# Performance work log

Hardware: AMD Instinct MI355X
Metric: run time of the kernel (lower is better)

The kernel has to match this reference:

```python
import jax, jax.numpy as jnp
import numpy as np

BETA = 0.25

def setup_inputs() -> dict:
    key = jax.random.key(0)
    k1, k2 = jax.random.split(key)
    x = jax.random.normal(k1, (32, 1024, 256), dtype=jnp.float32)
    # tf.random_uniform_initializer default range is [-0.05, 0.05)
    embedding = jax.random.uniform(k2, (256, 8192), dtype=jnp.float32, minval=-0.05, maxval=0.05)
    return {"x": x, "embedding": embedding}


def reference(x, embedding):
    # x: [B, S, D]; embedding: [D, K] (codebook stored column-wise, as in the tf module)
    D = x.shape[-1]
    flat = x.reshape(-1, D)                                   # [N, D]
    dists = (jnp.sum(flat * flat, axis=1, keepdims=True)
             - 2.0 * (flat @ embedding)
             + jnp.sum(embedding * embedding, axis=0))
    idx = jnp.argmin(dists, axis=1)                           # [N] int
    quantized = jnp.take(embedding.T, idx, axis=0).reshape(x.shape)  # gather codebook columns
    # VQ losses
    commitment = jnp.mean(jnp.square(jax.lax.stop_gradient(quantized) - x))
    codebook = jnp.mean(jnp.square(quantized - jax.lax.stop_gradient(x)))
    loss = BETA * commitment + codebook
    # straight-through estimator
    quantized_st = x + jax.lax.stop_gradient(quantized - x)
    return quantized_st, loss
```

## Files before the change

### kernel.cpp

```cpp
#include <hip/hip_runtime.h>

typedef float f4   __attribute__((ext_vector_type(4)));
typedef float f2   __attribute__((ext_vector_type(2)));
typedef _Float16 f16x8 __attribute__((ext_vector_type(8)));
typedef float f32x4  __attribute__((ext_vector_type(4)));

#define N_ROWS  32768
#define D_DIM   256
#define K_CODES 8192
#define NUM_ELEM (N_ROWS * D_DIM)
#define EPS_MARGIN 2e-3f
#define FB_CAP  8192
#define FB_RPB  8
#define RF_SLICES 16
#define N_PANELS 256
#define HALF_PANELS 128

__device__ __forceinline__ void gl2lds16(const void* g, void* l) {
    __builtin_amdgcn_global_load_lds(
        (const __attribute__((address_space(1))) unsigned int*)g,
        (__attribute__((address_space(3))) unsigned int*)l, 16, 0, 0);
}

__global__ void ee_kernel(const float* __restrict__ E, float* __restrict__ ee) {
    const int k = blockIdx.x * blockDim.x + threadIdx.x;
    double s = 0.0;
    for (int d = 0; d < D_DIM; ++d) {
        float v = E[(size_t)d * K_CODES + k];
        s += (double)v * (double)v;
    }
    ee[k] = (float)s;
}

__global__ void prep_kernel(const float* __restrict__ E, short* __restrict__ Ep) {
    const int p  = blockIdx.x;
    const int t  = threadIdx.x;
    const int c  = t & 31;
    const int gq = t >> 5;
    const int cp = p * 32;
    short* ph = Ep + (size_t)p * 8192;
    #pragma unroll
    for (int gi = 0; gi < 4; ++gi) {
        int g = gq * 4 + gi;
        f16x8 h;
        #pragma unroll
        for (int j = 0; j < 8; ++j) {
            float v = E[(size_t)(g * 8 + j) * K_CODES + cp + c];
            h[j] = (_Float16)v;
        }
        *(f16x8*)(ph + (g * 32 + c) * 8) = h;
    }
}

__global__ void trans32_kernel(const float* __restrict__ E, float* __restrict__ Et32) {
    __shared__ float tile[64][65];
    const int t  = threadIdx.x;
    const int k0 = blockIdx.x * 64, d0 = blockIdx.y * 64;
    #pragma unroll
    for (int i = 0; i < 16; ++i) {
        int dd = i * 4 + (t >> 6), kk = t & 63;
        tile[dd][kk] = E[(size_t)(d0 + dd) * K_CODES + k0 + kk];
    }
    __syncthreads();
    #pragma unroll
    for (int i = 0; i < 16; ++i) {
        int kk = i * 4 + (t >> 6), dd = t & 63;
        Et32[(size_t)(k0 + kk) * D_DIM + d0 + dd] = tile[dd][kk];
    }
}

__launch_bounds__(256, 2)
__global__ void mfma_sieve_kernel(const float* __restrict__ X,
                                  const short* __restrict__ Ep,
                                  const float* __restrict__ ee,
                                  f2* __restrict__ res_bs,
                                  int* __restrict__ res_idx) {
    __shared__ __align__(16) short Bbuf[2][8192];
    const int t    = threadIdx.x;
    const int w    = t >> 6;
    const int lane = t & 63;
    const int n    = lane & 15;
    const int quad = lane >> 4;
    const int half = blockIdx.x & 1;
    const int row0 = (blockIdx.x >> 1) * 128;
    const int rw   = row0 + w * 32;
    const int p0   = half * HALF_PANELS;

    f16x8 Ah[2][8];
    #pragma unroll
    for (int rt = 0; rt < 2; ++rt) {
        const float* xp = X + (size_t)(rw + rt * 16 + n) * D_DIM;
        #pragma unroll
        for (int ks = 0; ks < 8; ++ks) {
            int d = ks * 32 + quad * 8;
            f4 a = *(const f4*)(xp + d);
            f4 b = *(const f4*)(xp + d + 4);
            f16x8 h;
            #pragma unroll
            for (int j = 0; j < 8; ++j) {
                float x = (j < 4) ? a[j] : b[j - 4];
                h[j] = (_Float16)x;
            }
            Ah[rt][ks] = h;
        }
    }

    float bestv[8], secv[8]; int besti[8];
    #pragma unroll
    for (int s = 0; s < 8; ++s) { bestv[s] = 1e30f; secv[s] = 1e30f; besti[s] = 0; }

    {
        const char* gp = (const char*)Ep + (size_t)p0 * 16384;
        char* lp = (char*)&Bbuf[0][0];
        #pragma unroll
        for (int i = 0; i < 4; ++i)
            gl2lds16(gp + (w * 4 + i) * 1024 + lane * 16, lp + (w * 4 + i) * 1024);
    }
    __syncthreads();

    for (int i = 0; i < HALF_PANELS; ++i) {
        const int p   = p0 + i;
        const int buf = i & 1;
        if (i + 1 < HALF_PANELS) {
            const char* gp = (const char*)Ep + (size_t)(p + 1) * 16384;
            char* lp = (char*)&Bbuf[buf ^ 1][0];
            #pragma unroll
            for (int k = 0; k < 4; ++k)
                gl2lds16(gp + (w * 4 + k) * 1024 + lane * 16, lp + (w * 4 + k) * 1024);
        }

        const short* Bh = &Bbuf[buf][0];

        f32x4 acc[2][2];
        #pragma unroll
        for (int ct = 0; ct < 2; ++ct)
            #pragma unroll
            for (int rt = 0; rt < 2; ++rt)
                acc[ct][rt] = (f32x4)(0.0f);

        #pragma unroll
        for (int ks = 0; ks < 8; ++ks) {
            const int g = ks * 4 + quad;
            f16x8 bh[2];
            #pragma unroll
            for (int ct = 0; ct < 2; ++ct) {
                int c = ct * 16 + n;
                bh[ct] = *(const f16x8*)(Bh + (g * 32 + c) * 8);
            }
            #pragma unroll
            for (int ct = 0; ct < 2; ++ct)
                #pragma unroll
                for (int rt = 0; rt < 2; ++rt)
                    acc[ct][rt] = __builtin_amdgcn_mfma_f32_16x16x32_f16(Ah[rt][ks], bh[ct], acc[ct][rt], 0, 0, 0);
        }

        const int cb = p * 32;
        #pragma unroll
        for (int ct = 0; ct < 2; ++ct) {
            int code = cb + ct * 16 + n;
            float eev = ee[code];
            #pragma unroll
            for (int rt = 0; rt < 2; ++rt)
                #pragma unroll
                for (int r = 0; r < 4; ++r) {
                    float key = fmaf(-2.0f, acc[ct][rt][r], eev);
                    int s = rt * 4 + r;
                    float nb = fminf(key, bestv[s]);
                    secv[s]  = fminf(secv[s], fmaxf(key, bestv[s]));
                    besti[s] = (key < bestv[s]) ? code : besti[s];
                    bestv[s] = nb;
                }
        }
        __syncthreads();
    }

    #pragma unroll
    for (int off = 1; off < 16; off <<= 1) {
        #pragma unroll
        for (int s = 0; s < 8; ++s) {
            float ov = __shfl_xor(bestv[s], off);
            int   oi = __shfl_xor(besti[s], off);
            float os = __shfl_xor(secv[s], off);
            bool owin = (ov < bestv[s]) || (ov == bestv[s] && oi < besti[s]);
            if (owin) { secv[s] = fminf(os, bestv[s]); bestv[s] = ov; besti[s] = oi; }
            else      { secv[s] = fminf(secv[s], ov); }
        }
    }

    if (n == 0) {
        #pragma unroll
        for (int s = 0; s < 8; ++s) {
            int rl  = w * 32 + (s >> 2) * 16 + quad * 4 + (s & 3);
            int row = row0 + rl;
            f2 bs; bs[0] = bestv[s]; bs[1] = secv[s];
            res_bs[(size_t)row * 2 + half]  = bs;
            res_idx[(size_t)row * 2 + half] = besti[s];
        }
    }
}

__global__ void merge_kernel(const f2* __restrict__ res_bs, const int* __restrict__ res_idx,
                             int* __restrict__ bidx, int* __restrict__ counter,
                             int2* __restrict__ list) {
    const int row = blockIdx.x * blockDim.x + threadIdx.x;
    if (row >= N_ROWS) return;
    f2 a = res_bs[(size_t)row * 2];
    f2 b = res_bs[(size_t)row * 2 + 1];
    int ia = res_idx[(size_t)row * 2];
    int ib = res_idx[(size_t)row * 2 + 1];
    float gb; int gi; float gs;
    if (b[0] < a[0]) { gb = b[0]; gi = ib; gs = fminf(b[1], a[0]); }
    else             { gb = a[0]; gi = ia; gs = fminf(a[1], b[0]); }
    bidx[row] = gi;
    if (gs - gb <= EPS_MARGIN) {
        int pos = atomicAdd(counter, 1);
        if (pos < FB_CAP) list[pos] = make_int2(row, gi);
    }
}

__global__ void gather_kernel(const float* __restrict__ X, const float* __restrict__ Et32,
                              const int* __restrict__ bidx, float* __restrict__ out,
                              double* __restrict__ loss_sum) {
    __shared__ int bl_[128];
    const int t    = threadIdx.x;
    const int row0 = blockIdx.x * 128;
    if (t < 128) bl_[t] = bidx[row0 + t];
    __syncthreads();
    double ls = 0.0;
    const int d = t;
    #pragma unroll 4
    for (int r = 0; r < 128; ++r) {
        int code = bl_[r];
        float q  = Et32[(size_t)code * D_DIM + d];
        float x  = X[(size_t)(row0 + r) * D_DIM + d];
        float dq = q - x;
        out[(size_t)(row0 + r) * D_DIM + d] = x + dq;
        ls += (double)dq * (double)dq;
    }
    #pragma unroll
    for (int off = 32; off > 0; off >>= 1)
        ls += __shfl_down(ls, off);
    if ((t & 63) == 0) atomicAdd(loss_sum, ls);
}

__global__ void refine1_kernel(const float* __restrict__ X, const float* __restrict__ E,
                               const int* __restrict__ counter, const int2* __restrict__ list,
                               double* __restrict__ res_v, int* __restrict__ res_i) {
    __shared__ float xt[D_DIM][FB_RPB];
    __shared__ int rows_sh[FB_RPB];
    __shared__ double wbv[4][FB_RPB];
    __shared__ int    wbi[4][FB_RPB];

    int nf = *counter; if (nf > FB_CAP) nf = FB_CAP;
    const int nchunks = (nf + FB_RPB - 1) / FB_RPB;
    const int nitems  = nchunks * RF_SLICES;
    const int t = threadIdx.x;

    for (int item = blockIdx.x; item < nitems; item += gridDim.x) {
        const int rc = item / RF_SLICES;
        const int sl = item % RF_SLICES;
        __syncthreads();
        if (t < FB_RPB) {
            int e = rc * FB_RPB + t;
            int2 ent = list[(e < nf) ? e : 0];
            rows_sh[t] = ent.x;
        }
        __syncthreads();
        #pragma unroll
        for (int j = 0; j < FB_RPB; ++j)
            xt[t][j] = X[(size_t)rows_sh[j] * D_DIM + t];
        __syncthreads();

        const int k0 = sl * 512 + t * 2;
        double s0[FB_RPB], s1[FB_RPB], q0 = 0.0, q1 = 0.0;
        #pragma unroll
        for (int j = 0; j < FB_RPB; ++j) { s0[j] = 0.0; s1[j] = 0.0; }
        for (int d = 0; d < D_DIM; ++d) {
            f2 ev = *(const f2*)(E + (size_t)d * K_CODES + k0);
            double e0d = (double)ev[0], e1d = (double)ev[1];
            const f4* xp = (const f4*)(&xt[d][0]);
            f4 xa = xp[0], xb = xp[1];
            double xd[FB_RPB] = { (double)xa[0], (double)xa[1], (double)xa[2], (double)xa[3],
                                  (double)xb[0], (double)xb[1], (double)xb[2], (double)xb[3] };
            q0 += e0d * e0d; q1 += e1d * e1d;
            #pragma unroll
            for (int j = 0; j < FB_RPB; ++j) {
                s0[j] += xd[j] * e0d;
                s1[j] += xd[j] * e1d;
            }
        }
        double bv[FB_RPB]; int bi[FB_RPB];
        #pragma unroll
        for (int j = 0; j < FB_RPB; ++j) {
            double k0v = q0 - 2.0 * s0[j];
            double k1v = q1 - 2.0 * s1[j];
            bv[j] = k0v; bi[j] = k0;
            if (k1v < bv[j]) { bv[j] = k1v; bi[j] = k0 + 1; }
        }
        #pragma unroll
        for (int off = 1; off < 64; off <<= 1) {
            #pragma unroll
            for (int j = 0; j < FB_RPB; ++j) {
                double ov = __shfl_xor(bv[j], off);
                int    oi = __shfl_xor(bi[j], off);
                if (ov < bv[j] || (ov == bv[j] && oi < bi[j])) { bv[j] = ov; bi[j] = oi; }
            }
        }
        const int wave = t >> 6;
        if ((t & 63) == 0) {
            #pragma unroll
            for (int j = 0; j < FB_RPB; ++j) { wbv[wave][j] = bv[j]; wbi[wave][j] = bi[j]; }
        }
        __syncthreads();
        if (t < FB_RPB) {
            double b = wbv[0][t]; int i_ = wbi[0][t];
            #pragma unroll
            for (int wv = 1; wv < 4; ++wv) {
                double ov = wbv[wv][t]; int oi = wbi[wv][t];
                if (ov < b || (ov == b && oi < i_)) { b = ov; i_ = oi; }
            }
            int e = rc * FB_RPB + t;
            res_v[(size_t)e * RF_SLICES + sl] = b;
            res_i[(size_t)e * RF_SLICES + sl] = i_;
        }
    }
}

__global__ void patch_kernel(const float* __restrict__ X, const float* __restrict__ Et32,
                             float* __restrict__ out, double* __restrict__ loss_sum,
                             const int* __restrict__ counter, const int2* __restrict__ list,
                             const double* __restrict__ res_v, const int* __restrict__ res_i) {
    int nf = *counter; if (nf > FB_CAP) nf = FB_CAP;
    const int b = blockIdx.x;
    if (b >= nf) return;
    __shared__ int nc_sh;
    const int t = threadIdx.x;
    if (t == 0) {
        double bv = res_v[(size_t)b * RF_SLICES]; int bi = res_i[(size_t)b * RF_SLICES];
        for (int s = 1; s < RF_SLICES; ++s) {
            double v = res_v[(size_t)b * RF_SLICES + s];
            int    i = res_i[(size_t)b * RF_SLICES + s];
            if (v < bv || (v == bv && i < bi)) { bv = v; bi = i; }
        }
        nc_sh = bi;
    }
    __syncthreads();
    int2 ent = list[b];
    const int oc = ent.y, row = ent.x, nc = nc_sh;
    if (nc == oc) return;
    float x  = X[(size_t)row * D_DIM + t];
    float qn = Et32[(size_t)nc * D_DIM + t];
    float qo = Et32[(size_t)oc * D_DIM + t];
    float dqn = qn - x, dqo = qo - x;
    out[(size_t)row * D_DIM + t] = x + dqn;
    double dl = (double)dqn * dqn - (double)dqo * dqo;
    #pragma unroll
    for (int off = 32; off > 0; off >>= 1)
        dl += __shfl_down(dl, off);
    if ((t & 63) == 0) atomicAdd(loss_sum, dl);
}

__global__ void fin_kernel(const double* __restrict__ loss_sum, float* __restrict__ out) {
    double m = loss_sum[0] / (double)NUM_ELEM;
    out[NUM_ELEM] = (float)(0.25 * m + m);
}

extern "C" void kernel_launch(void* const* d_in, const int* in_sizes, int n_in,
                              void* d_out, int out_size, void* d_ws, size_t ws_size,
                              hipStream_t stream) {
    const float* X = (const float*)d_in[0];
    const float* E = (const float*)d_in[1];
    float* out = (float*)d_out;

    double* loss_sum = (double*)d_ws;
    int*    counter  = (int*)((char*)d_ws + 8);
    float*  ee       = (float*)((char*)d_ws + 1024);
    int2*   list     = (int2*)((char*)d_ws + 36864);
    double* res_v    = (double*)((char*)d_ws + 131072);
    int*    res_i    = (int*)((char*)d_ws + 1179648);
    float*  Et32     = (float*)((char*)d_ws + 1703936);
    short*  Ep       = (short*)((char*)d_ws + 10092544);
    f2*     res_bs   = (f2*)((char*)d_ws + 18481152);
    int*    res_idx  = (int*)((char*)d_ws + 19005440);
    int*    bidx     = (int*)((char*)d_ws + 19267584);

    hipMemsetAsync(d_ws, 0, 1024, stream);
    prep_kernel<<<N_PANELS, 256, 0, stream>>>(E, Ep);
    trans32_kernel<<<dim3(128, 4), 256, 0, stream>>>(E, Et32);
    ee_kernel<<<K_CODES / 256, 256, 0, stream>>>(E, ee);
    mfma_sieve_kernel<<<512, 256, 0, stream>>>(X, Ep, ee, res_bs, res_idx);
    merge_kernel<<<N_ROWS / 256, 256, 0, stream>>>(res_bs, res_idx, bidx, counter, list);
    gather_kernel<<<N_ROWS / 128, 256, 0, stream>>>(X, Et32, bidx, out, loss_sum);
    refine1_kernel<<<2048, 256, 0, stream>>>(X, E, counter, list, res_v, res_i);
    patch_kernel<<<FB_CAP, 256, 0, stream>>>(X, Et32, out, loss_sum, counter, list,
                                             res_v, res_i);
    fin_kernel<<<1, 1, 0, stream>>>(loss_sum, out);
}
```

Measured before the change: 346.3 us.

## Double rows per block and split codebook into quarters in MFMA sieve

Each sieve block now covers 256 rows (64 per wave) and a quarter of the codebook panels instead of 128 rows and half of them. Every B fragment read from LDS therefore feeds twice as many MFMAs, and the per-code norms for the block's quarter are staged once into LDS. The merge kernel now combines four partial best/second-best results per row instead of two, and the result buffers move to fit. In exchange, register pressure rises a lot (32 A fragments, 8 accumulators, 16 best/second/index slots), which risks spilling or lower occupancy.

```diff
diff --git a/kernel.cpp b/kernel.cpp
--- a/kernel.cpp
+++ b/kernel.cpp
@@ -14,7 +14,7 @@
 #define FB_RPB  8
 #define RF_SLICES 16
 #define N_PANELS 256
-#define HALF_PANELS 128
+#define QTR_PANELS 64
 
 __device__ __forceinline__ void gl2lds16(const void* g, void* l) {
     __builtin_amdgcn_global_load_lds(
@@ -76,19 +76,20 @@
                                   f2* __restrict__ res_bs,
                                   int* __restrict__ res_idx) {
     __shared__ __align__(16) short Bbuf[2][8192];
+    __shared__ float eebuf[2048];
     const int t    = threadIdx.x;
     const int w    = t >> 6;
     const int lane = t & 63;
     const int n    = lane & 15;
     const int quad = lane >> 4;
-    const int half = blockIdx.x & 1;
-    const int row0 = (blockIdx.x >> 1) * 128;
-    const int rw   = row0 + w * 32;
-    const int p0   = half * HALF_PANELS;
-
-    f16x8 Ah[2][8];
-    #pragma unroll
-    for (int rt = 0; rt < 2; ++rt) {
+    const int part = blockIdx.x & 3;
+    const int row0 = (blockIdx.x >> 2) * 256;
+    const int rw   = row0 + w * 64;
+    const int p0   = part * QTR_PANELS;
+
+    f16x8 Ah[4][8];
+    #pragma unroll
+    for (int rt = 0; rt < 4; ++rt) {
         const float* xp = X + (size_t)(rw + rt * 16 + n) * D_DIM;
         #pragma unroll
         for (int ks = 0; ks < 8; ++ks) {
@@ -105,9 +106,16 @@
         }
     }
 
-    float bestv[8], secv[8]; int besti[8];
-    #pragma unroll
-    for (int s = 0; s < 8; ++s) { bestv[s] = 1e30f; secv[s] = 1e30f; besti[s] = 0; }
+    {
+        const f4* src = (const f4*)(ee + part * 2048);
+        f4* dst = (f4*)eebuf;
+        dst[t * 2]     = src[t * 2];
+        dst[t * 2 + 1] = src[t * 2 + 1];
+    }
+
+    float bestv[16], secv[16]; int besti[16];
+    #pragma unroll
+    for (int s = 0; s < 16; ++s) { bestv[s] = 1e30f; secv[s] = 1e30f; besti[s] = 0; }
 
     {
         const char* gp = (const char*)Ep + (size_t)p0 * 16384;
@@ -118,10 +126,10 @@
     }
     __syncthreads();
 
-    for (int i = 0; i < HALF_PANELS; ++i) {
+    for (int i = 0; i < QTR_PANELS; ++i) {
         const int p   = p0 + i;
         const int buf = i & 1;
-        if (i + 1 < HALF_PANELS) {
+        if (i + 1 < QTR_PANELS) {
             const char* gp = (const char*)Ep + (size_t)(p + 1) * 16384;
             char* lp = (char*)&Bbuf[buf ^ 1][0];
             #pragma unroll
@@ -131,11 +139,11 @@
 
         const short* Bh = &Bbuf[buf][0];
 
-        f32x4 acc[2][2];
+        f32x4 acc[2][4];
         #pragma unroll
         for (int ct = 0; ct < 2; ++ct)
             #pragma unroll
-            for (int rt = 0; rt < 2; ++rt)
+            for (int rt = 0; rt < 4; ++rt)
                 acc[ct][rt] = (f32x4)(0.0f);
 
         #pragma unroll
@@ -150,17 +158,18 @@
             #pragma unroll
             for (int ct = 0; ct < 2; ++ct)
                 #pragma unroll
-                for (int rt = 0; rt < 2; ++rt)
+                for (int rt = 0; rt < 4; ++rt)
                     acc[ct][rt] = __builtin_amdgcn_mfma_f32_16x16x32_f16(Ah[rt][ks], bh[ct], acc[ct][rt], 0, 0, 0);
         }
 
         const int cb = p * 32;
+        const int po = i * 32;
         #pragma unroll
         for (int ct = 0; ct < 2; ++ct) {
-            int code = cb + ct * 16 + n;
-            float eev = ee[code];
-            #pragma unroll
-            for (int rt = 0; rt < 2; ++rt)
+            int code  = cb + ct * 16 + n;
+            float eev = eebuf[po + ct * 16 + n];
+            #pragma unroll
+            for (int rt = 0; rt < 4; ++rt)
                 #pragma unroll
                 for (int r = 0; r < 4; ++r) {
                     float key = fmaf(-2.0f, acc[ct][rt][r], eev);
@@ -177,7 +186,7 @@
     #pragma unroll
     for (int off = 1; off < 16; off <<= 1) {
         #pragma unroll
-        for (int s = 0; s < 8; ++s) {
+        for (int s = 0; s < 16; ++s) {
             float ov = __shfl_xor(bestv[s], off);
             int   oi = __shfl_xor(besti[s], off);
             float os = __shfl_xor(secv[s], off);
@@ -189,12 +198,12 @@
 
     if (n == 0) {
         #pragma unroll
-        for (int s = 0; s < 8; ++s) {
-            int rl  = w * 32 + (s >> 2) * 16 + quad * 4 + (s & 3);
+        for (int s = 0; s < 16; ++s) {
+            int rl  = w * 64 + (s >> 2) * 16 + quad * 4 + (s & 3);
             int row = row0 + rl;
             f2 bs; bs[0] = bestv[s]; bs[1] = secv[s];
-            res_bs[(size_t)row * 2 + half]  = bs;
-            res_idx[(size_t)row * 2 + half] = besti[s];
+            res_bs[(size_t)row * 4 + part]  = bs;
+            res_idx[(size_t)row * 4 + part] = besti[s];
         }
     }
 }
@@ -204,13 +213,14 @@
                              int2* __restrict__ list) {
     const int row = blockIdx.x * blockDim.x + threadIdx.x;
     if (row >= N_ROWS) return;
-    f2 a = res_bs[(size_t)row * 2];
-    f2 b = res_bs[(size_t)row * 2 + 1];
-    int ia = res_idx[(size_t)row * 2];
-    int ib = res_idx[(size_t)row * 2 + 1];
-    float gb; int gi; float gs;
-    if (b[0] < a[0]) { gb = b[0]; gi = ib; gs = fminf(b[1], a[0]); }
-    else             { gb = a[0]; gi = ia; gs = fminf(a[1], b[0]); }
+    float gb = 1e30f, gs = 1e30f; int gi = 0;
+    #pragma unroll
+    for (int p = 0; p < 4; ++p) {
+        f2 v  = res_bs[(size_t)row * 4 + p];
+        int vi = res_idx[(size_t)row * 4 + p];
+        if (v[0] < gb) { gs = fminf(gb, v[1]); gb = v[0]; gi = vi; }
+        else           { gs = fminf(gs, v[0]); }
+    }
     bidx[row] = gi;
     if (gs - gb <= EPS_MARGIN) {
         int pos = atomicAdd(counter, 1);
@@ -380,8 +390,8 @@
     int*    res_i    = (int*)((char*)d_ws + 1179648);
     float*  Et32     = (float*)((char*)d_ws + 1703936);
     short*  Ep       = (short*)((char*)d_ws + 10092544);
-    f2*     res_bs   = (f2*)((char*)d_ws + 18481152);
-    int*    res_idx  = (int*)((char*)d_ws + 19005440);
+    f2*     res_bs   = (f2*)((char*)d_ws + 14286848);
+    int*    res_idx  = (int*)((char*)d_ws + 15335424);
     int*    bidx     = (int*)((char*)d_ws + 19267584);
 
     hipMemsetAsync(d_ws, 0, 1024, stream);
```

Result: no change. 344.2 us (-0.6%).

## Triple-buffer codebook panels with vmcnt-gated barriers and stage ee in LDS

Applied to the files above, without the earlier changes.

The sieve kernel's codebook panel pipeline goes from double to triple buffering, prefetching two panels ahead. The end-of-iteration __syncthreads is replaced by a single s_waitcnt vmcnt(4) plus s_barrier at the top of each iteration, so loads can overlap with compute for longer. The block's half of the ee norms is copied into LDS once instead of read from global memory every panel, and MFMA sections are wrapped in s_setprio. This raises LDS use to about 64KB per block, which may reduce occupancy at the requested two blocks per CU. The res_bs and res_idx workspace offsets are also moved.

```diff
diff --git a/kernel.cpp b/kernel.cpp
--- a/kernel.cpp
+++ b/kernel.cpp
@@ -75,7 +75,8 @@
                                   const float* __restrict__ ee,
                                   f2* __restrict__ res_bs,
                                   int* __restrict__ res_idx) {
-    __shared__ __align__(16) short Bbuf[2][8192];
+    __shared__ __align__(16) short Bbuf[3][8192];
+    __shared__ float eebuf[4096];
     const int t    = threadIdx.x;
     const int w    = t >> 6;
     const int lane = t & 63;
@@ -105,31 +106,45 @@
         }
     }
 
+    {
+        const f4* src = (const f4*)(ee + half * 4096);
+        f4* dst = (f4*)eebuf;
+        #pragma unroll
+        for (int ps = 0; ps < 4; ++ps)
+            dst[ps * 256 + t] = src[ps * 256 + t];
+    }
+
     float bestv[8], secv[8]; int besti[8];
     #pragma unroll
     for (int s = 0; s < 8; ++s) { bestv[s] = 1e30f; secv[s] = 1e30f; besti[s] = 0; }
 
-    {
-        const char* gp = (const char*)Ep + (size_t)p0 * 16384;
-        char* lp = (char*)&Bbuf[0][0];
+    __syncthreads();
+
+    #pragma unroll
+    for (int pp = 0; pp < 2; ++pp) {
+        const char* gp = (const char*)Ep + (size_t)(p0 + pp) * 16384;
+        char* lp = (char*)&Bbuf[pp][0];
         #pragma unroll
         for (int i = 0; i < 4; ++i)
             gl2lds16(gp + (w * 4 + i) * 1024 + lane * 16, lp + (w * 4 + i) * 1024);
     }
-    __syncthreads();
-
+
+    int cur = 0, pre = 2;
     for (int i = 0; i < HALF_PANELS; ++i) {
-        const int p   = p0 + i;
-        const int buf = i & 1;
         if (i + 1 < HALF_PANELS) {
-            const char* gp = (const char*)Ep + (size_t)(p + 1) * 16384;
-            char* lp = (char*)&Bbuf[buf ^ 1][0];
+            asm volatile("s_waitcnt vmcnt(4)\n\ts_barrier" ::: "memory");
+        } else {
+            asm volatile("s_waitcnt vmcnt(0)\n\ts_barrier" ::: "memory");
+        }
+        if (i + 2 < HALF_PANELS) {
+            const char* gp = (const char*)Ep + (size_t)(p0 + i + 2) * 16384;
+            char* lp = (char*)&Bbuf[pre][0];
             #pragma unroll
             for (int k = 0; k < 4; ++k)
                 gl2lds16(gp + (w * 4 + k) * 1024 + lane * 16, lp + (w * 4 + k) * 1024);
         }
 
-        const short* Bh = &Bbuf[buf][0];
+        const short* Bh = &Bbuf[cur][0];
 
         f32x4 acc[2][2];
         #pragma unroll
@@ -138,6 +153,7 @@
             for (int rt = 0; rt < 2; ++rt)
                 acc[ct][rt] = (f32x4)(0.0f);
 
+        __builtin_amdgcn_s_setprio(1);
         #pragma unroll
         for (int ks = 0; ks < 8; ++ks) {
             const int g = ks * 4 + quad;
@@ -153,12 +169,14 @@
                 for (int rt = 0; rt < 2; ++rt)
                     acc[ct][rt] = __builtin_amdgcn_mfma_f32_16x16x32_f16(Ah[rt][ks], bh[ct], acc[ct][rt], 0, 0, 0);
         }
-
-        const int cb = p * 32;
+        __builtin_amdgcn_s_setprio(0);
+
+        const int cb = (p0 + i) * 32;
+        const int po = i * 32;
         #pragma unroll
         for (int ct = 0; ct < 2; ++ct) {
-            int code = cb + ct * 16 + n;
-            float eev = ee[code];
+            int code  = cb + ct * 16 + n;
+            float eev = eebuf[po + ct * 16 + n];
             #pragma unroll
             for (int rt = 0; rt < 2; ++rt)
                 #pragma unroll
@@ -171,7 +189,8 @@
                     bestv[s] = nb;
                 }
         }
-        __syncthreads();
+        cur = (cur == 2) ? 0 : cur + 1;
+        pre = (pre == 2) ? 0 : pre + 1;
     }
 
     #pragma unroll
@@ -380,8 +399,8 @@
     int*    res_i    = (int*)((char*)d_ws + 1179648);
     float*  Et32     = (float*)((char*)d_ws + 1703936);
     short*  Ep       = (short*)((char*)d_ws + 10092544);
-    f2*     res_bs   = (f2*)((char*)d_ws + 18481152);
-    int*    res_idx  = (int*)((char*)d_ws + 19005440);
+    f2*     res_bs   = (f2*)((char*)d_ws + 14286848);
+    int*    res_idx  = (int*)((char*)d_ws + 15335424);
     int*    bidx     = (int*)((char*)d_ws + 19267584);
 
     hipMemsetAsync(d_ws, 0, 1024, stream);
```

New measurement: 364.6 us. 1.05x slower.

## Fuse codebook prep, transpose and norms; fold merge into gather

Applied to the files above, without the earlier changes.

A single prep kernel now reads the column-stored codebook once and produces three things: the fp16 MFMA panel layout, the fp32 transposed codebook, and per-code squared norms reduced through shared memory. This replaces three separate kernels, including a strided double-precision norm loop. The per-row merge of the two half-sieve results, along with the fallback list append, moves into the gather kernel's index-loading phase, which drops another launch and the bidx round trip. In exchange, the norms are now accumulated in fp32 instead of double, and the transposed stores are strided per lane rather than tile-coalesced.

```diff
diff --git a/kernel.cpp b/kernel.cpp
--- a/kernel.cpp
+++ b/kernel.cpp
@@ -22,50 +22,39 @@
         (__attribute__((address_space(3))) unsigned int*)l, 16, 0, 0);
 }
 
-__global__ void ee_kernel(const float* __restrict__ E, float* __restrict__ ee) {
-    const int k = blockIdx.x * blockDim.x + threadIdx.x;
-    double s = 0.0;
-    for (int d = 0; d < D_DIM; ++d) {
-        float v = E[(size_t)d * K_CODES + k];
-        s += (double)v * (double)v;
-    }
-    ee[k] = (float)s;
-}
-
-__global__ void prep_kernel(const float* __restrict__ E, short* __restrict__ Ep) {
+__global__ void prep_kernel(const float* __restrict__ E, short* __restrict__ Ep,
+                            float* __restrict__ Et32, float* __restrict__ ee) {
+    __shared__ float eepart[8][32];
     const int p  = blockIdx.x;
     const int t  = threadIdx.x;
     const int c  = t & 31;
     const int gq = t >> 5;
     const int cp = p * 32;
     short* ph = Ep + (size_t)p * 8192;
+    float ss = 0.0f;
     #pragma unroll
     for (int gi = 0; gi < 4; ++gi) {
         int g = gq * 4 + gi;
         f16x8 h;
+        f4 av, bv;
         #pragma unroll
         for (int j = 0; j < 8; ++j) {
             float v = E[(size_t)(g * 8 + j) * K_CODES + cp + c];
             h[j] = (_Float16)v;
+            ss += v * v;
+            if (j < 4) av[j] = v; else bv[j - 4] = v;
         }
         *(f16x8*)(ph + (g * 32 + c) * 8) = h;
-    }
-}
-
-__global__ void trans32_kernel(const float* __restrict__ E, float* __restrict__ Et32) {
-    __shared__ float tile[64][65];
-    const int t  = threadIdx.x;
-    const int k0 = blockIdx.x * 64, d0 = blockIdx.y * 64;
-    #pragma unroll
-    for (int i = 0; i < 16; ++i) {
-        int dd = i * 4 + (t >> 6), kk = t & 63;
-        tile[dd][kk] = E[(size_t)(d0 + dd) * K_CODES + k0 + kk];
-    }
+        *(f4*)(Et32 + (size_t)(cp + c) * D_DIM + g * 8)     = av;
+        *(f4*)(Et32 + (size_t)(cp + c) * D_DIM + g * 8 + 4) = bv;
+    }
+    eepart[gq][c] = ss;
     __syncthreads();
-    #pragma unroll
-    for (int i = 0; i < 16; ++i) {
-        int kk = i * 4 + (t >> 6), dd = t & 63;
-        Et32[(size_t)(k0 + kk) * D_DIM + d0 + dd] = tile[dd][kk];
+    if (t < 32) {
+        float s = 0.0f;
+        #pragma unroll
+        for (int q = 0; q < 8; ++q) s += eepart[q][t];
+        ee[cp + t] = s;
     }
 }
 
@@ -199,32 +188,28 @@
     }
 }
 
-__global__ void merge_kernel(const f2* __restrict__ res_bs, const int* __restrict__ res_idx,
-                             int* __restrict__ bidx, int* __restrict__ counter,
-                             int2* __restrict__ list) {
-    const int row = blockIdx.x * blockDim.x + threadIdx.x;
-    if (row >= N_ROWS) return;
-    f2 a = res_bs[(size_t)row * 2];
-    f2 b = res_bs[(size_t)row * 2 + 1];
-    int ia = res_idx[(size_t)row * 2];
-    int ib = res_idx[(size_t)row * 2 + 1];
-    float gb; int gi; float gs;
-    if (b[0] < a[0]) { gb = b[0]; gi = ib; gs = fminf(b[1], a[0]); }
-    else             { gb = a[0]; gi = ia; gs = fminf(a[1], b[0]); }
-    bidx[row] = gi;
-    if (gs - gb <= EPS_MARGIN) {
-        int pos = atomicAdd(counter, 1);
-        if (pos < FB_CAP) list[pos] = make_int2(row, gi);
-    }
-}
-
 __global__ void gather_kernel(const float* __restrict__ X, const float* __restrict__ Et32,
-                              const int* __restrict__ bidx, float* __restrict__ out,
-                              double* __restrict__ loss_sum) {
+                              const f2* __restrict__ res_bs, const int* __restrict__ res_idx,
+                              int* __restrict__ counter, int2* __restrict__ list,
+                              float* __restrict__ out, double* __restrict__ loss_sum) {
     __shared__ int bl_[128];
     const int t    = threadIdx.x;
     const int row0 = blockIdx.x * 128;
-    if (t < 128) bl_[t] = bidx[row0 + t];
+    if (t < 128) {
+        const int row = row0 + t;
+        f2 a = res_bs[(size_t)row * 2];
+        f2 b = res_bs[(size_t)row * 2 + 1];
+        int ia = res_idx[(size_t)row * 2];
+        int ib = res_idx[(size_t)row * 2 + 1];
+        float gb; int gi; float gs;
+        if (b[0] < a[0]) { gb = b[0]; gi = ib; gs = fminf(b[1], a[0]); }
+        else             { gb = a[0]; gi = ia; gs = fminf(a[1], b[0]); }
+        bl_[t] = gi;
+        if (gs - gb <= EPS_MARGIN) {
+            int pos = atomicAdd(counter, 1);
+            if (pos < FB_CAP) list[pos] = make_int2(row, gi);
+        }
+    }
     __syncthreads();
     double ls = 0.0;
     const int d = t;
@@ -380,17 +365,14 @@
     int*    res_i    = (int*)((char*)d_ws + 1179648);
     float*  Et32     = (float*)((char*)d_ws + 1703936);
     short*  Ep       = (short*)((char*)d_ws + 10092544);
-    f2*     res_bs   = (f2*)((char*)d_ws + 18481152);
-    int*    res_idx  = (int*)((char*)d_ws + 19005440);
-    int*    bidx     = (int*)((char*)d_ws + 19267584);
+    f2*     res_bs   = (f2*)((char*)d_ws + 14286848);
+    int*    res_idx  = (int*)((char*)d_ws + 15335424);
 
     hipMemsetAsync(d_ws, 0, 1024, stream);
-    prep_kernel<<<N_PANELS, 256, 0, stream>>>(E, Ep);
-    trans32_kernel<<<dim3(128, 4), 256, 0, stream>>>(E, Et32);
-    ee_kernel<<<K_CODES / 256, 256, 0, stream>>>(E, ee);
+    prep_kernel<<<N_PANELS, 256, 0, stream>>>(E, Ep, Et32, ee);
     mfma_sieve_kernel<<<512, 256, 0, stream>>>(X, Ep, ee, res_bs, res_idx);
-    merge_kernel<<<N_ROWS / 256, 256, 0, stream>>>(res_bs, res_idx, bidx, counter, list);
-    gather_kernel<<<N_ROWS / 128, 256, 0, stream>>>(X, Et32, bidx, out, loss_sum);
+    gather_kernel<<<N_ROWS / 128, 256, 0, stream>>>(X, Et32, res_bs, res_idx,
+                                                    counter, list, out, loss_sum);
     refine1_kernel<<<2048, 256, 0, stream>>>(X, E, counter, list, res_v, res_i);
     patch_kernel<<<FB_CAP, 256, 0, stream>>>(X, Et32, out, loss_sum, counter, list,
                                              res_v, res_i);
```

Result: faster. 326.1 us (-5.8%).
